# Performance work log

Hardware: AMD Instinct MI355X
Metric: run time of the kernel (lower is better)

Reference implementation:

```python
import jax, jax.numpy as jnp
import numpy as np

B, T, D = 4, 2048, 1024
N_HEADS = 16
HEAD_DIM = D // N_HEADS


def setup_inputs() -> dict:
    key = jax.random.key(0)
    ks = jax.random.split(key, 12)
    s = 1.0 / np.sqrt(D)
    return {
        "query": jax.random.normal(ks[0], (B, T, D), jnp.float32),
        "key_value": jax.random.normal(ks[1], (B, T, D), jnp.float32),
        "Wq": jax.random.uniform(ks[2], (D, D), jnp.float32, -s, s),
        "bq": jax.random.uniform(ks[3], (D,), jnp.float32, -s, s),
        "Wk": jax.random.uniform(ks[4], (D, D), jnp.float32, -s, s),
        "bk": jax.random.uniform(ks[5], (D,), jnp.float32, -s, s),
        "Wv": jax.random.uniform(ks[6], (D, D), jnp.float32, -s, s),
        "bv": jax.random.uniform(ks[7], (D,), jnp.float32, -s, s),
        "Wo": jax.random.uniform(ks[8], (D, D), jnp.float32, -s, s),
        "bo": jax.random.uniform(ks[9], (D,), jnp.float32, -s, s),
        "lookahead": 128,
    }


def reference(query, key_value, Wq, bq, Wk, bk, Wv, bv, Wo, bo, lookahead):
    b, t, d = query.shape
    scale = HEAD_DIM ** -0.5
    # projections: [B,T,D] -> [B,H,T,hd]
    def split_heads(x):
        return x.reshape(b, t, N_HEADS, HEAD_DIM).transpose(0, 2, 1, 3)
    Q = split_heads(query @ Wq.T + bq)
    K = split_heads(key_value @ Wk.T + bk)
    V = split_heads(key_value @ Wv.T + bv)
    # banded causal mask: key j allowed iff j <= i + lookahead
    i = jnp.arange(t)[:, None]
    j = jnp.arange(t)[None, :]
    allowed = j <= i + lookahead  # [T,T] bool
    scores = jnp.einsum('bhqd,bhkd->bhqk', Q, K) * scale
    scores = jnp.where(allowed, scores, -jnp.inf)
    attn = jax.nn.softmax(scores, axis=-1)  # dropout p=0.0 (eval)
    out = jnp.einsum('bhqk,bhkd->bhqd', attn, V)
    out = out.transpose(0, 2, 1, 3).reshape(b, t, d)
    return out @ Wo.T + bo
```

## Files before the change

kernel.cpp:

```cpp
#include <hip/hip_runtime.h>
#include <hip/hip_bf16.h>

typedef __attribute__((ext_vector_type(8))) short short8;
typedef __attribute__((ext_vector_type(4))) float f32x4;
typedef __attribute__((ext_vector_type(16))) float f32x16;

#define LOG2E 1.44269504088896340736f

__global__ __launch_bounds__(256) void k_cvtX(const float* __restrict__ q_in,
                                              const float* __restrict__ kv_in,
                                              __hip_bfloat16* __restrict__ Xq) {
  int i = blockIdx.x * blockDim.x + threadIdx.x;
  const int stride = gridDim.x * blockDim.x;
  for (; i < 4194304; i += stride) {
    const float4 v = (i < 2097152) ? reinterpret_cast<const float4*>(q_in)[i]
                                   : reinterpret_cast<const float4*>(kv_in)[i - 2097152];
    union { __hip_bfloat16 h[4]; short4 s; } p;
    p.h[0] = __float2bfloat16(v.x);
    p.h[1] = __float2bfloat16(v.y);
    p.h[2] = __float2bfloat16(v.z);
    p.h[3] = __float2bfloat16(v.w);
    reinterpret_cast<short4*>(Xq)[i] = p.s;
  }
}

__global__ __launch_bounds__(256) void k_cvtW(const float* __restrict__ Wq,
                                              const float* __restrict__ Wk,
                                              const float* __restrict__ Wv,
                                              const float* __restrict__ Wo,
                                              __hip_bfloat16* __restrict__ Wqkv,
                                              __hip_bfloat16* __restrict__ Wob) {
  int i = blockIdx.x * blockDim.x + threadIdx.x;
  const int stride = gridDim.x * blockDim.x;
  for (; i < 1048576; i += stride) {
    float4 v;
    short4* dst;
    if (i < 786432) {
      const float4* src = (i < 262144) ? reinterpret_cast<const float4*>(Wq)
                         : (i < 524288) ? reinterpret_cast<const float4*>(Wk)
                                        : reinterpret_cast<const float4*>(Wv);
      v = src[i & 262143];
      dst = reinterpret_cast<short4*>(Wqkv) + i;
    } else {
      v = reinterpret_cast<const float4*>(Wo)[i - 786432];
      dst = reinterpret_cast<short4*>(Wob) + (i - 786432);
    }
    union { __hip_bfloat16 h[4]; short4 s; } p;
    p.h[0] = __float2bfloat16(v.x);
    p.h[1] = __float2bfloat16(v.y);
    p.h[2] = __float2bfloat16(v.z);
    p.h[3] = __float2bfloat16(v.w);
    *dst = p.s;
  }
}

__device__ __forceinline__ void gload_lds16(const __hip_bfloat16* g, __hip_bfloat16* l) {
  __builtin_amdgcn_global_load_lds(
      (const __attribute__((address_space(1))) unsigned int*)g,
      (__attribute__((address_space(3))) unsigned int*)l, 16, 0, 0);
}

__device__ __forceinline__ unsigned pk_bf16(float a, float b) {
  union { __hip_bfloat16 h; unsigned short u; } x, y;
  x.h = __float2bfloat16(a);
  y.h = __float2bfloat16(b);
  return (unsigned)x.u | ((unsigned)y.u << 16);
}

__device__ __forceinline__ void plswap2(unsigned a, unsigned b, unsigned& x, unsigned& y) {
#if __has_builtin(__builtin_amdgcn_permlane32_swap)
  auto r = __builtin_amdgcn_permlane32_swap(a, b, false, false);
  x = r[0];
  y = r[1];
#else
  unsigned d, s;
  asm volatile("v_mov_b32 %0, %2\n\tv_mov_b32 %1, %3\n\tv_permlane32_swap_b32 %0, %1"
               : "=&v"(d), "=&v"(s)
               : "v"(a), "v"(b));
  x = d;
  y = s;
#endif
}

template <int NB, int OUTMODE>
__global__ __launch_bounds__(256, 4) void k_gemm(
    const __hip_bfloat16* __restrict__ Aq, const __hip_bfloat16* __restrict__ Akv,
    const __hip_bfloat16* __restrict__ Wt,
    const float* __restrict__ b0p, const float* __restrict__ b1p, const float* __restrict__ b2p,
    __hip_bfloat16* __restrict__ Obf, float* __restrict__ Of) {
  const int K = 1024;
  __shared__ __hip_bfloat16 As[4][4096];
  __shared__ __hip_bfloat16 Bs[4][4096];
  const int tid = threadIdx.x;
  const int lane = tid & 63;
  const int w = tid >> 6;
  const int wr = w >> 1, wc = w & 1;
  const int lg = lane >> 4, lr = lane & 15;

  const int bid = blockIdx.x;
  const int xcd = bid & 7, idx = bid >> 3;
  const int m0 = (xcd * 8 + idx / NB) * 128;
  const int n0 = (idx % NB) * 128;

  const int proj = (OUTMODE == 0) ? (n0 >> 10) : 0;
  const __hip_bfloat16* A = (OUTMODE == 0) ? (proj == 0 ? Aq : Akv) : Aq;

  const f32x4 fzero = {0.f, 0.f, 0.f, 0.f};
  f32x4 acc[4][4];
#pragma unroll
  for (int i = 0; i < 4; i++)
#pragma unroll
    for (int j = 0; j < 4; j++) acc[i][j] = fzero;

  const int c0 = w * 2;
  const int srow = lane >> 2;
  const int scol = (lane & 3) * 8;

  auto STAGE = [&](int kt, int buf) {
    const int k0 = kt * 32;
#pragma unroll
    for (int i = 0; i < 2; i++) {
      const int c = c0 + i;
      const int row = c * 16 + srow;
      gload_lds16(A + (size_t)(m0 + row) * K + k0 + scol, As[buf] + c * 512);
      gload_lds16(Wt + (size_t)(n0 + row) * K + k0 + scol, Bs[buf] + c * 512);
    }
  };

  STAGE(0, 0);
  STAGE(1, 1);

  for (int kt = 0; kt < 32; ++kt) {
    if (kt + 2 < 32) {
      STAGE(kt + 2, (kt + 2) & 3);
      asm volatile("s_waitcnt vmcnt(8)" ::: "memory");
    } else if (kt + 1 < 32) {
      asm volatile("s_waitcnt vmcnt(4)" ::: "memory");
    } else {
      asm volatile("s_waitcnt vmcnt(0)" ::: "memory");
    }
    __builtin_amdgcn_s_barrier();

    const int bc = kt & 3;
    short8 af[4], bfr[4];
#pragma unroll
    for (int mi = 0; mi < 4; mi++)
      af[mi] = *(const short8*)(As[bc] + (wr * 64 + mi * 16 + lr) * 32 + lg * 8);
#pragma unroll
    for (int ni = 0; ni < 4; ni++)
      bfr[ni] = *(const short8*)(Bs[bc] + (wc * 64 + ni * 16 + lr) * 32 + lg * 8);
#pragma unroll
    for (int mi = 0; mi < 4; mi++)
#pragma unroll
      for (int ni = 0; ni < 4; ni++)
        acc[mi][ni] = __builtin_amdgcn_mfma_f32_16x16x32_bf16(af[mi], bfr[ni], acc[mi][ni], 0, 0, 0);
  }

  const float scale = (OUTMODE == 0 && proj == 0) ? (0.125f * LOG2E) : 1.0f;
  const float* bias = (OUTMODE == 0) ? (proj == 0 ? b0p : (proj == 1 ? b1p : b2p)) : b0p;
  __hip_bfloat16* Ob = (OUTMODE == 0) ? (Obf + (size_t)proj * 8388608) : nullptr;

#pragma unroll
  for (int mi = 0; mi < 4; mi++) {
#pragma unroll
    for (int ni = 0; ni < 4; ni++) {
      const int n = n0 + wc * 64 + ni * 16 + lr;
      const float bn = bias[n & 1023];
#pragma unroll
      for (int r = 0; r < 4; r++) {
        const int m = m0 + wr * 64 + mi * 16 + lg * 4 + r;
        const float v = (acc[mi][ni][r] + bn) * scale;
        if (OUTMODE == 0) {
          const int b = m >> 11, t = m & 2047;
          const int h = (n >> 6) & 15, d = n & 63;
          Ob[(((size_t)(b * 16 + h)) * 2048 + t) * 64 + d] = __float2bfloat16(v);
        } else {
          Of[(size_t)m * 1024 + n] = v;
        }
      }
    }
  }
}

__global__ __launch_bounds__(256) void k_transpose(const __hip_bfloat16* __restrict__ V,
                                                   __hip_bfloat16* __restrict__ Vt) {
  __shared__ __hip_bfloat16 tile[64][72];
  const int bh = blockIdx.y;
  const int t0 = blockIdx.x * 64;
  const int tid = threadIdx.x;
#pragma unroll
  for (int it = 0; it < 2; ++it) {
    const int r = it * 32 + (tid >> 3);
    const int c = (tid & 7) * 8;
    short8 v = *(const short8*)(V + ((size_t)bh * 2048 + t0 + r) * 64 + c);
    *(short8*)(&tile[r][c]) = v;
  }
  __syncthreads();
#pragma unroll
  for (int it = 0; it < 2; ++it) {
    const int d = it * 32 + (tid >> 3);
    const int tt = (tid & 7) * 8;
    __hip_bfloat16 tmp[8];
#pragma unroll
    for (int j = 0; j < 8; j++) tmp[j] = tile[tt + j][d];
    *(short8*)(Vt + ((size_t)bh * 64 + d) * 2048 + t0 + tt) = *(short8*)tmp;
  }
}

__global__ __launch_bounds__(256, 5) void k_attn4(const __hip_bfloat16* __restrict__ Qm,
                                                  const __hip_bfloat16* __restrict__ Km,
                                                  const __hip_bfloat16* __restrict__ Vt,
                                                  __hip_bfloat16* __restrict__ O,
                                                  const int* __restrict__ la_ptr) {
  const int T = 2048;
  __shared__ __hip_bfloat16 Ks[2][4096];
  __shared__ __hip_bfloat16 Vs[2][4096];
  const int tid = threadIdx.x;
  const int lane = tid & 63;
  const int w = tid >> 6;
  const int hi = lane >> 5;
  const int l31 = lane & 31;

  const int l = blockIdx.y * 16 + blockIdx.x;
  const int half = l >> 9;
  const int u = l & 511;
  const int xi = u & 15;
  const int yi = u >> 4;
  const int qblk = half ? (15 - xi) : xi;
  const int bh = yi + (half << 5);

  const int q0 = qblk * 128;
  const int la = *la_ptr;
  const int qw = q0 + w * 32;
  const int q = qw + l31;

  short8 qf[4];
  {
    const __hip_bfloat16* qrow = Qm + ((size_t)bh * T + q) * 64;
#pragma unroll
    for (int ks = 0; ks < 4; ks++) qf[ks] = *(const short8*)(qrow + ks * 16 + hi * 8);
  }

  f32x16 acc0, acc1;
#pragma unroll
  for (int r = 0; r < 16; r++) { acc0[r] = 0.f; acc1[r] = 0.f; }
  float lsum = 0.f;

  const int kend_w = min(T, qw + 32 + la);
  const int kend_b = min(T, q0 + 128 + la);
  const int ntiles = (kend_b + 63) >> 6;

  const int srow = tid >> 3;
  const int sc16 = (tid & 7) ^ (srow & 7);
  const __hip_bfloat16* Kg = Km + (size_t)bh * T * 64 + (size_t)srow * 64 + sc16 * 8;
  const __hip_bfloat16* Vg = Vt + (size_t)bh * 64 * T + (size_t)srow * T + sc16 * 8;
  const int kswz = l31 & 7;

  auto STAGEKV = [&](int t, int buf) {
    const size_t koffg = (size_t)(t << 6) * 64;
    gload_lds16(Kg + koffg, Ks[buf] + w * 512);
    gload_lds16(Kg + koffg + 32 * 64, Ks[buf] + 2048 + w * 512);
    gload_lds16(Vg + (t << 6), Vs[buf] + w * 512);
    gload_lds16(Vg + (t << 6) + (size_t)32 * T, Vs[buf] + 2048 + w * 512);
  };

  STAGEKV(0, 0);

  int cur = 0;
  for (int kt = 0; kt < ntiles; ++kt) {
    const int kbase = kt << 6;
    if (kt + 1 < ntiles) {
      STAGEKV(kt + 1, cur ^ 1);
      asm volatile("s_waitcnt vmcnt(4)" ::: "memory");
    } else {
      asm volatile("s_waitcnt vmcnt(0)" ::: "memory");
    }
    __syncthreads();

    if (kbase < kend_w) {
      const __hip_bfloat16* Ksc = Ks[cur];
      const __hip_bfloat16* Vsc = Vs[cur];
#pragma unroll
      for (int kt2 = 0; kt2 < 2; ++kt2) {
        const int kb32 = kbase + kt2 * 32;
        if (kb32 >= kend_w) break;
        const int krow = kt2 * 32 + l31;

        f32x16 s;
#pragma unroll
        for (int r = 0; r < 16; r++) s[r] = 0.f;
#pragma unroll
        for (int ks = 0; ks < 4; ks++) {
          short8 kf = *(const short8*)((const char*)Ksc + krow * 128 +
                                       ((((ks << 1) | hi)) ^ kswz) * 16);
          s = __builtin_amdgcn_mfma_f32_32x32x16_bf16(kf, qf[ks], s, 0, 0, 0);
        }

        if (kb32 + 31 > qw + la) {
          const int thr = q + la - kb32;
#pragma unroll
          for (int r = 0; r < 16; r++) {
            const int crow = (r & 3) + ((r >> 2) << 3) + (hi << 2);
            if (crow > thr) s[r] = -1e30f;
          }
        }

        float ps = 0.f;
        unsigned W[8];
#pragma unroll
        for (int i = 0; i < 8; i++) {
          const float ea = exp2f(s[2 * i]);
          const float eb = exp2f(s[2 * i + 1]);
          ps += ea + eb;
          W[i] = pk_bf16(ea, eb);
        }
        lsum += ps;

        int4 A0, A1;
        {
          unsigned x0, z0, y0, w0, x1, z1, y1, w1;
          plswap2(W[0], W[2], x0, z0);
          plswap2(W[1], W[3], y0, w0);
          plswap2(W[4], W[6], x1, z1);
          plswap2(W[5], W[7], y1, w1);
          A0.x = (int)x0; A0.y = (int)y0; A0.z = (int)z0; A0.w = (int)w0;
          A1.x = (int)x1; A1.y = (int)y1; A1.z = (int)z1; A1.w = (int)w1;
        }

#pragma unroll
        for (int ks2 = 0; ks2 < 2; ks2++) {
          union { int4 i; short8 s8; } pa;
          pa.i = ks2 ? A1 : A0;
          const int ksg = kt2 * 2 + ks2;
          const int col16 = ((ksg << 1) | hi);
          short8 vf0 = *(const short8*)((const char*)Vsc + l31 * 128 + ((col16 ^ kswz)) * 16);
          short8 vf1 = *(const short8*)((const char*)Vsc + (32 + l31) * 128 + ((col16 ^ kswz)) * 16);
          acc0 = __builtin_amdgcn_mfma_f32_32x32x16_bf16(vf0, pa.s8, acc0, 0, 0, 0);
          acc1 = __builtin_amdgcn_mfma_f32_32x32x16_bf16(vf1, pa.s8, acc1, 0, 0, 0);
        }
      }
    }
    __syncthreads();
    cur ^= 1;
  }

  {
    unsigned r0, r1;
    plswap2(__float_as_uint(lsum), __float_as_uint(lsum), r0, r1);
    lsum = __uint_as_float(r0) + __uint_as_float(r1);
  }
  const float rinv = 1.f / lsum;
  const int b = bh >> 4, h = bh & 15;
  __hip_bfloat16* orow = O + ((size_t)(b * T + q)) * 1024 + h * 64;
#pragma unroll
  for (int rq = 0; rq < 4; rq++) {
    const int d0 = rq * 8 + hi * 4;
    union { __hip_bfloat16 h4[4]; short4 s4; } o;
#pragma unroll
    for (int j = 0; j < 4; j++) o.h4[j] = __float2bfloat16(acc0[rq * 4 + j] * rinv);
    *(short4*)(orow + d0) = o.s4;
  }
#pragma unroll
  for (int rq = 0; rq < 4; rq++) {
    const int d0 = rq * 8 + hi * 4 + 32;
    union { __hip_bfloat16 h4[4]; short4 s4; } o;
#pragma unroll
    for (int j = 0; j < 4; j++) o.h4[j] = __float2bfloat16(acc1[rq * 4 + j] * rinv);
    *(short4*)(orow + d0) = o.s4;
  }
}

extern "C" void kernel_launch(void* const* d_in, const int* in_sizes, int n_in,
                              void* d_out, int out_size, void* d_ws, size_t ws_size,
                              hipStream_t stream) {
  const float* q_in = (const float*)d_in[0];
  const float* kv_in = (const float*)d_in[1];
  const float* Wq = (const float*)d_in[2];
  const float* bq = (const float*)d_in[3];
  const float* Wk = (const float*)d_in[4];
  const float* bk = (const float*)d_in[5];
  const float* Wv = (const float*)d_in[6];
  const float* bv = (const float*)d_in[7];
  const float* Wo = (const float*)d_in[8];
  const float* bo = (const float*)d_in[9];
  const int* la = (const int*)d_in[10];

  char* ws = (char*)d_ws;
  const size_t SZX = (size_t)8192 * 1024 * 2;
  const size_t SZW = (size_t)1024 * 1024 * 2;
  __hip_bfloat16* Xq = (__hip_bfloat16*)(ws);
  __hip_bfloat16* Xkv = (__hip_bfloat16*)(ws + SZX);
  __hip_bfloat16* Wqkv = (__hip_bfloat16*)(ws + 2 * SZX);
  __hip_bfloat16* Wob = (__hip_bfloat16*)(ws + 2 * SZX + 3 * SZW);
  __hip_bfloat16* Qb = (__hip_bfloat16*)(ws + 2 * SZX + 4 * SZW);
  __hip_bfloat16* Kb = (__hip_bfloat16*)(ws + 3 * SZX + 4 * SZW);
  __hip_bfloat16* Vb = (__hip_bfloat16*)(ws + 4 * SZX + 4 * SZW);
  __hip_bfloat16* Vtb = (__hip_bfloat16*)(ws);
  __hip_bfloat16* AOb = (__hip_bfloat16*)(ws + SZX);

  k_cvtX<<<4096, 256, 0, stream>>>(q_in, kv_in, Xq);
  k_cvtW<<<2048, 256, 0, stream>>>(Wq, Wk, Wv, Wo, Wqkv, Wob);

  k_gemm<24, 0><<<1536, 256, 0, stream>>>(Xq, Xkv, Wqkv, bq, bk, bv, Qb, nullptr);
  k_transpose<<<dim3(32, 64), 256, 0, stream>>>(Vb, Vtb);
  k_attn4<<<dim3(16, 64), 256, 0, stream>>>(Qb, Kb, Vtb, AOb, la);
  k_gemm<8, 1><<<512, 256, 0, stream>>>(AOb, AOb, Wob, bo, bo, bo, nullptr, (float*)d_out);

  (void)Kb;
}
```

Before: 234.0 us.

## Triple-buffer K/V tiles in attention, drop trailing barrier, batch QK MFMAs

The attention kernel moves from a double to a triple LDS ring buffer for K and V. This lets it drop the second __syncthreads per tile, and the top barrier becomes a raw s_barrier. Both 32-key QK^T score blocks are now computed before either softmax/PV step, giving the scheduler more independent MFMA work to overlap with the exp and pack code, and the row-sum reduction is restructured as a tree. Occupancy hint drops from 5 to 3 blocks per CU because LDS use grows by half. The mapping of q-block order across halves is also flipped.

```diff
diff --git a/kernel.cpp b/kernel.cpp
--- a/kernel.cpp
+++ b/kernel.cpp
@@ -207,14 +207,14 @@
   }
 }
 
-__global__ __launch_bounds__(256, 5) void k_attn4(const __hip_bfloat16* __restrict__ Qm,
+__global__ __launch_bounds__(256, 3) void k_attn5(const __hip_bfloat16* __restrict__ Qm,
                                                   const __hip_bfloat16* __restrict__ Km,
                                                   const __hip_bfloat16* __restrict__ Vt,
                                                   __hip_bfloat16* __restrict__ O,
                                                   const int* __restrict__ la_ptr) {
   const int T = 2048;
-  __shared__ __hip_bfloat16 Ks[2][4096];
-  __shared__ __hip_bfloat16 Vs[2][4096];
+  __shared__ __hip_bfloat16 Ks[3][4096];
+  __shared__ __hip_bfloat16 Vs[3][4096];
   const int tid = threadIdx.x;
   const int lane = tid & 63;
   const int w = tid >> 6;
@@ -226,7 +226,7 @@
   const int u = l & 511;
   const int xi = u & 15;
   const int yi = u >> 4;
-  const int qblk = half ? (15 - xi) : xi;
+  const int qblk = half ? xi : (15 - xi);
   const int bh = yi + (half << 5);
 
   const int q0 = qblk * 128;
@@ -264,84 +264,90 @@
     gload_lds16(Vg + (t << 6) + (size_t)32 * T, Vs[buf] + 2048 + w * 512);
   };
 
+  auto QK = [&](const __hip_bfloat16* Ksc, int kt2) {
+    const int krow = kt2 * 32 + l31;
+    f32x16 s;
+#pragma unroll
+    for (int r = 0; r < 16; r++) s[r] = 0.f;
+#pragma unroll
+    for (int ks = 0; ks < 4; ks++) {
+      short8 kf = *(const short8*)((const char*)Ksc + krow * 128 +
+                                   ((((ks << 1) | hi)) ^ kswz) * 16);
+      s = __builtin_amdgcn_mfma_f32_32x32x16_bf16(kf, qf[ks], s, 0, 0, 0);
+    }
+    return s;
+  };
+
+  auto SMPV = [&](f32x16& s, int kb32, int kt2, const __hip_bfloat16* Vsc) {
+    if (kb32 + 31 > qw + la) {
+      const int thr = q + la - kb32;
+#pragma unroll
+      for (int r = 0; r < 16; r++) {
+        const int crow = (r & 3) + ((r >> 2) << 3) + (hi << 2);
+        if (crow > thr) s[r] = -1e30f;
+      }
+    }
+    float e[16];
+#pragma unroll
+    for (int i = 0; i < 16; i++) e[i] = exp2f(s[i]);
+    float p01 = (e[0] + e[1]) + (e[2] + e[3]);
+    float p23 = (e[4] + e[5]) + (e[6] + e[7]);
+    float p45 = (e[8] + e[9]) + (e[10] + e[11]);
+    float p67 = (e[12] + e[13]) + (e[14] + e[15]);
+    lsum += (p01 + p23) + (p45 + p67);
+    unsigned W[8];
+#pragma unroll
+    for (int i = 0; i < 8; i++) W[i] = pk_bf16(e[2 * i], e[2 * i + 1]);
+
+    int4 A0, A1;
+    {
+      unsigned x0, z0, y0, w0, x1, z1, y1, w1;
+      plswap2(W[0], W[2], x0, z0);
+      plswap2(W[1], W[3], y0, w0);
+      plswap2(W[4], W[6], x1, z1);
+      plswap2(W[5], W[7], y1, w1);
+      A0.x = (int)x0; A0.y = (int)y0; A0.z = (int)z0; A0.w = (int)w0;
+      A1.x = (int)x1; A1.y = (int)y1; A1.z = (int)z1; A1.w = (int)w1;
+    }
+
+#pragma unroll
+    for (int ks2 = 0; ks2 < 2; ks2++) {
+      union { int4 i; short8 s8; } pa;
+      pa.i = ks2 ? A1 : A0;
+      const int ksg = kt2 * 2 + ks2;
+      const int col16 = ((ksg << 1) | hi);
+      short8 vf0 = *(const short8*)((const char*)Vsc + l31 * 128 + ((col16 ^ kswz)) * 16);
+      short8 vf1 = *(const short8*)((const char*)Vsc + (32 + l31) * 128 + ((col16 ^ kswz)) * 16);
+      acc0 = __builtin_amdgcn_mfma_f32_32x32x16_bf16(vf0, pa.s8, acc0, 0, 0, 0);
+      acc1 = __builtin_amdgcn_mfma_f32_32x32x16_bf16(vf1, pa.s8, acc1, 0, 0, 0);
+    }
+  };
+
   STAGEKV(0, 0);
 
-  int cur = 0;
+  int cur = 0, nxt = 1;
   for (int kt = 0; kt < ntiles; ++kt) {
     const int kbase = kt << 6;
     if (kt + 1 < ntiles) {
-      STAGEKV(kt + 1, cur ^ 1);
+      STAGEKV(kt + 1, nxt);
       asm volatile("s_waitcnt vmcnt(4)" ::: "memory");
     } else {
       asm volatile("s_waitcnt vmcnt(0)" ::: "memory");
     }
-    __syncthreads();
+    __builtin_amdgcn_s_barrier();
 
     if (kbase < kend_w) {
       const __hip_bfloat16* Ksc = Ks[cur];
       const __hip_bfloat16* Vsc = Vs[cur];
-#pragma unroll
-      for (int kt2 = 0; kt2 < 2; ++kt2) {
-        const int kb32 = kbase + kt2 * 32;
-        if (kb32 >= kend_w) break;
-        const int krow = kt2 * 32 + l31;
-
-        f32x16 s;
-#pragma unroll
-        for (int r = 0; r < 16; r++) s[r] = 0.f;
-#pragma unroll
-        for (int ks = 0; ks < 4; ks++) {
-          short8 kf = *(const short8*)((const char*)Ksc + krow * 128 +
-                                       ((((ks << 1) | hi)) ^ kswz) * 16);
-          s = __builtin_amdgcn_mfma_f32_32x32x16_bf16(kf, qf[ks], s, 0, 0, 0);
-        }
-
-        if (kb32 + 31 > qw + la) {
-          const int thr = q + la - kb32;
-#pragma unroll
-          for (int r = 0; r < 16; r++) {
-            const int crow = (r & 3) + ((r >> 2) << 3) + (hi << 2);
-            if (crow > thr) s[r] = -1e30f;
-          }
-        }
-
-        float ps = 0.f;
-        unsigned W[8];
-#pragma unroll
-        for (int i = 0; i < 8; i++) {
-          const float ea = exp2f(s[2 * i]);
-          const float eb = exp2f(s[2 * i + 1]);
-          ps += ea + eb;
-          W[i] = pk_bf16(ea, eb);
-        }
-        lsum += ps;
-
-        int4 A0, A1;
-        {
-          unsigned x0, z0, y0, w0, x1, z1, y1, w1;
-          plswap2(W[0], W[2], x0, z0);
-          plswap2(W[1], W[3], y0, w0);
-          plswap2(W[4], W[6], x1, z1);
-          plswap2(W[5], W[7], y1, w1);
-          A0.x = (int)x0; A0.y = (int)y0; A0.z = (int)z0; A0.w = (int)w0;
-          A1.x = (int)x1; A1.y = (int)y1; A1.z = (int)z1; A1.w = (int)w1;
-        }
-
-#pragma unroll
-        for (int ks2 = 0; ks2 < 2; ks2++) {
-          union { int4 i; short8 s8; } pa;
-          pa.i = ks2 ? A1 : A0;
-          const int ksg = kt2 * 2 + ks2;
-          const int col16 = ((ksg << 1) | hi);
-          short8 vf0 = *(const short8*)((const char*)Vsc + l31 * 128 + ((col16 ^ kswz)) * 16);
-          short8 vf1 = *(const short8*)((const char*)Vsc + (32 + l31) * 128 + ((col16 ^ kswz)) * 16);
-          acc0 = __builtin_amdgcn_mfma_f32_32x32x16_bf16(vf0, pa.s8, acc0, 0, 0, 0);
-          acc1 = __builtin_amdgcn_mfma_f32_32x32x16_bf16(vf1, pa.s8, acc1, 0, 0, 0);
-        }
-      }
-    }
-    __syncthreads();
-    cur ^= 1;
+      const bool d1 = (kbase + 32) < kend_w;
+      f32x16 sA = QK(Ksc, 0);
+      f32x16 sB;
+      if (d1) sB = QK(Ksc, 1);
+      SMPV(sA, kbase, 0, Vsc);
+      if (d1) SMPV(sB, kbase + 32, 1, Vsc);
+    }
+    cur = nxt;
+    nxt = (nxt == 2) ? 0 : nxt + 1;
   }
 
   {
@@ -403,7 +409,7 @@
 
   k_gemm<24, 0><<<1536, 256, 0, stream>>>(Xq, Xkv, Wqkv, bq, bk, bv, Qb, nullptr);
   k_transpose<<<dim3(32, 64), 256, 0, stream>>>(Vb, Vtb);
-  k_attn4<<<dim3(16, 64), 256, 0, stream>>>(Qb, Kb, Vtb, AOb, la);
+  k_attn5<<<dim3(16, 64), 256, 0, stream>>>(Qb, Kb, Vtb, AOb, la);
   k_gemm<8, 1><<<512, 256, 0, stream>>>(AOb, AOb, Wob, bo, bo, bo, nullptr, (float*)d_out);
 
   (void)Kb;
```

New measurement: 234.0 us. About the same (+0.0%).
